# Optimization experiments

Measured on AMD Instinct MI355X. Metric: run time of the kernel, lower is better.

The kernel has to match this reference:

```python
import jax, jax.numpy as jnp
import numpy as np

NB, NC, NT = 64, 128, 6
NEURON = (25, 50, 100)
AXIS = 4
EPS = 1e-12


def _offdiag_idx(nc):
    # static [nc, nc-1] column indices of the off-diagonal entries per row
    idx = np.tile(np.arange(nc)[None, :], (nc, 1))
    mask = ~np.eye(nc, dtype=bool)
    return idx[mask].reshape(nc, nc - 1)


def setup_inputs() -> dict:
    key = jax.random.key(0)
    ks = jax.random.split(key, 8)
    P = NT * NT
    coords = jax.random.normal(ks[0], (NB, NC, 3), dtype=jnp.float32)
    atom_types = jax.random.randint(ks[1], (NC,), 0, NT)
    dims = [1] + list(NEURON)
    inp = {"coords": coords, "atom_types": atom_types}
    for i in range(3):
        bound = 1.0 / float(np.sqrt(dims[i]))
        inp[f"W{i+1}"] = jax.random.uniform(ks[2 + 2 * i], (P, dims[i + 1], dims[i]), jnp.float32, -bound, bound)
        inp[f"b{i+1}"] = jax.random.uniform(ks[3 + 2 * i], (P, dims[i + 1]), jnp.float32, -bound, bound)
    return inp


def _channel_dense(x, W, b, channels, res_mode):
    # x: [nb, Ppairs, in]; W[channels]: [Ppairs, out, in] (redundant per-pair gather, as in torch)
    y = jnp.einsum('bpi,poi->bpo', x, W[channels]) + b[channels]
    y = jnp.tanh(y)
    if res_mode == 1:
        y = y + x
    elif res_mode == 2:
        y = y + jnp.concatenate([x, x], axis=-1)
    return y


def _forward(coords, atom_types, W1, b1, W2, b2, W3, b3):
    nb, nc, _ = coords.shape
    idx = jnp.asarray(_offdiag_idx(nc))  # [nc, nc-1], static
    row = jnp.arange(nc)[:, None]

    rij = coords[:, :, None, :] - coords[:, None, :, :]          # [nb,nc,nc,3]
    rij = rij[:, row, idx]                                       # [nb,nc,nc-1,3] off-diagonal
    dij = jnp.linalg.norm(rij, axis=-1)                          # [nb,nc,nc-1]
    dinv = 1.0 / jnp.maximum(dij, EPS)
    loc_env_r = dinv
    loc_env_a = rij * (dinv * dinv)[..., None]                   # [nb,nc,nc-1,3]

    neighbor_types = atom_types[idx]                             # [nc,nc-1]
    channels = (atom_types[:, None] * NT + neighbor_types).reshape(-1)  # [nc*(nc-1)]

    x = loc_env_r.reshape(nb, -1, 1)                             # [nb,P,1]
    y = _channel_dense(x, W1, b1, channels, res_mode=0)          # 1 -> 25
    y = _channel_dense(y, W2, b2, channels, res_mode=2)          # 25 -> 50 (+concat res)
    y = _channel_dense(y, W3, b3, channels, res_mode=2)          # 50 -> 100 (+concat res)

    out = y.reshape(nb, nc, nc - 1, NEURON[-1])                  # [nb,nc,k,100]
    t1 = jnp.einsum('bnka,bnkf->bnaf', loc_env_a, out[..., :AXIS])   # [nb,nc,3,4]
    t2 = jnp.einsum('bnka,bnaf->bnkf', loc_env_a, t1)                # [nb,nc,k,4]
    res = jnp.einsum('bnkg,bnkf->bngf', out, t2)                     # [nb,nc,100,4]
    return res.reshape(nb, nc, -1)


def reference(coords, atom_types, W1, b1, W2, b2, W3, b3):
    return _forward(coords, atom_types, W1, b1, W2, b2, W3, b3)
```

## Files before the change

### kernel.cpp

```cpp
#include <hip/hip_runtime.h>

#define NBATCH 64
#define NCH    128
#define NTYPE  6
#define NK     127
#define N1     25
#define N2     50
#define N3     100
#define NAXIS  4
#define OUTPER 400
#define W2P    28
#define MAXKP  152
#define MAXC4  38

#define R5(M)  M(0) M(1) M(2) M(3) M(4)
#define R7(M)  M(0) M(1) M(2) M(3) M(4) M(5) M(6)
#define R12(M) M(0) M(1) M(2) M(3) M(4) M(5) M(6) M(7) M(8) M(9) M(10) M(11)
#define R25(M) M(0) M(1) M(2) M(3) M(4) M(5) M(6) M(7) M(8) M(9) M(10) M(11) M(12) \
               M(13) M(14) M(15) M(16) M(17) M(18) M(19) M(20) M(21) M(22) M(23) M(24)
#define R25A(M,a) M(a,0) M(a,1) M(a,2) M(a,3) M(a,4) M(a,5) M(a,6) M(a,7) M(a,8) M(a,9) \
               M(a,10) M(a,11) M(a,12) M(a,13) M(a,14) M(a,15) M(a,16) M(a,17) M(a,18) \
               M(a,19) M(a,20) M(a,21) M(a,22) M(a,23) M(a,24)
#define R50(M) R25(M) M(25) M(26) M(27) M(28) M(29) M(30) M(31) M(32) M(33) M(34) \
               M(35) M(36) M(37) M(38) M(39) M(40) M(41) M(42) M(43) M(44) M(45) \
               M(46) M(47) M(48) M(49)

__device__ __forceinline__ float tanh_fast(float x) {
    float e = __expf(2.0f * x);
    return 1.0f - 2.0f * __builtin_amdgcn_rcpf(e + 1.0f);
}

__global__ void k_transpose(const float* __restrict__ coords, float* __restrict__ ct) {
    int t = blockIdx.x * blockDim.x + threadIdx.x;
    if (t >= NBATCH * NCH * 3) return;
    int b  = t & (NBATCH - 1);
    int jd = t >> 6;
    int d  = jd % 3;
    int j  = jd / 3;
    ct[t] = coords[(b * NCH + j) * 3 + d];
}

__device__ __forceinline__ void sort_k_by_type(
    const int* __restrict__ types, int n, int* tysh, int* ks, int* bins, int tid, int nthr)
{
    for (int t = tid; t < NCH; t += nthr) tysh[t] = types[t];
    __syncthreads();
    if (tid == 0) {
        for (int t = 0; t < NTYPE; ++t) bins[t] = 0;
        for (int k = 0; k < NK; ++k) { int j = (k < n) ? k : k + 1; bins[tysh[j]]++; }
        int off = 0;
        for (int t = 0; t < NTYPE; ++t) { int c = bins[t]; bins[t] = off; off += c; }
        for (int k = 0; k < NK; ++k) { int j = (k < n) ? k : k + 1; ks[bins[tysh[j]]++] = k; }
    }
    __syncthreads();
}

__device__ __forceinline__ void sort_pad(
    const int* __restrict__ types, int n, int* tysh, int* ksp, int* chs, int* aux,
    int tid, int nthr)
{
    for (int t = tid; t < NCH; t += nthr) tysh[t] = types[t];
    __syncthreads();
    if (tid == 0) {
        int cnt[NTYPE], pos[NTYPE];
        for (int t = 0; t < NTYPE; ++t) cnt[t] = 0;
        for (int k = 0; k < NK; ++k) { int j = (k < n) ? k : k + 1; cnt[tysh[j]]++; }
        int c = 0;
        for (int t = 0; t < NTYPE; ++t) {
            pos[t] = c;
            int pc = (cnt[t] + 3) & ~3;
            for (int q = c >> 2; q < (c + pc) >> 2; ++q) chs[q] = t;
            for (int p = c + cnt[t]; p < c + pc; ++p) ksp[p] = -1;
            c += pc;
        }
        aux[0] = c >> 2;
        for (int k = 0; k < NK; ++k) { int j = (k < n) ? k : k + 1; ksp[pos[tysh[j]]++] = k; }
    }
    __syncthreads();
}

__global__ __launch_bounds__(256, 4) void k_mlp(
    const float* __restrict__ ct, const int* __restrict__ types,
    const float* __restrict__ W1, const float* __restrict__ B1,
    const float* __restrict__ W2, const float* __restrict__ B2,
    const float* __restrict__ W3, const float* __restrict__ B3,
    float* __restrict__ t1buf)
{
    __shared__ int ks[NK];
    __shared__ int tysh[NCH];
    __shared__ int bins[NTYPE];

    const int n  = blockIdx.x >> 2;
    const int qc = blockIdx.x & 3;
    const int w  = threadIdx.x >> 6;
    const int b  = threadIdx.x & 63;
    const int k0 = qc * 32 + w * 8;

    sort_k_by_type(types, n, tysh, ks, bins, threadIdx.x, 256);

    const float cx = ct[(n*3+0)*NBATCH + b];
    const float cy = ct[(n*3+1)*NBATCH + b];
    const float cz = ct[(n*3+2)*NBATCH + b];
    const int tn = __builtin_amdgcn_readfirstlane(tysh[n]);

    float t1a[12];
#define TIN(i) t1a[i] = 0.0f;
    R12(TIN)
#undef TIN

    for (int kk = 0; kk < 8; ++kk) {
        const int kidx = k0 + kk;
        if (kidx >= NK) break;
        const int sk = __builtin_amdgcn_readfirstlane(ks[kidx]);
        const int j  = (sk < n) ? sk : sk + 1;
        const int ch = __builtin_amdgcn_readfirstlane(tn * NTYPE + tysh[j]);

        const float dx = cx - ct[(j*3+0)*NBATCH + b];
        const float dy = cy - ct[(j*3+1)*NBATCH + b];
        const float dz = cz - ct[(j*3+2)*NBATCH + b];
        const float d2 = dx*dx + dy*dy + dz*dz;
        const float dd = sqrtf(d2);
        const float dinv = __builtin_amdgcn_rcpf(fmaxf(dd, 1e-12f));
        const float di2 = dinv * dinv;
        const float ax = dx * di2, ay = dy * di2, az = dz * di2;

        const float* w1r = W1 + ch * N1;
        const float* b1r = B1 + ch * N1;
        float y1[N1];
#define L1S(o) y1[o] = tanh_fast(fmaf(dinv, w1r[o], b1r[o]));
        R25(L1S)
#undef L1S

        const float* w2r = W2 + ch * (N2 * N1);
        const float* b2r = B2 + ch * N2;
        const float* w3r = W3 + ch * (N3 * N2);
        float zf[4];
        zf[0] = B3[ch*N3+0]; zf[1] = B3[ch*N3+1];
        zf[2] = B3[ch*N3+2]; zf[3] = B3[ch*N3+3];
        float r[4];
#define MLP2I(o,i) z = fmaf(w2r[(o)*N1+(i)], y1[i], z);
#define MLP2(o) { float z = b2r[o]; R25A(MLP2I,o) \
        float y2o = tanh_fast(z) + y1[(o)%N1]; \
        if ((o) < 4) r[(o)&3] = y2o; \
        zf[0] = fmaf(w3r[0*N2+(o)], y2o, zf[0]); \
        zf[1] = fmaf(w3r[1*N2+(o)], y2o, zf[1]); \
        zf[2] = fmaf(w3r[2*N2+(o)], y2o, zf[2]); \
        zf[3] = fmaf(w3r[3*N2+(o)], y2o, zf[3]); }
        R50(MLP2)
#undef MLP2
#undef MLP2I

#define O4F(f) { float o4 = tanh_fast(zf[f]) + r[f]; \
        t1a[0+(f)] = fmaf(ax, o4, t1a[0+(f)]); \
        t1a[4+(f)] = fmaf(ay, o4, t1a[4+(f)]); \
        t1a[8+(f)] = fmaf(az, o4, t1a[8+(f)]); }
        O4F(0) O4F(1) O4F(2) O4F(3)
#undef O4F
    }

    float* dst = t1buf + (n * 12) * NBATCH + b;
#define TAT(i) atomicAdd(dst + (i) * NBATCH, t1a[i]);
    R12(TAT)
#undef TAT
}

__global__ __launch_bounds__(512, 3) void k_res2(
    const float* __restrict__ ct, const int* __restrict__ types,
    const float* __restrict__ W1, const float* __restrict__ B1,
    const float* __restrict__ W2, const float* __restrict__ B2,
    const float* __restrict__ W3, const float* __restrict__ B3,
    const float* __restrict__ t1buf, float* __restrict__ out)
{
    __shared__ float y2t[4 * N2 * NBATCH];
    __shared__ float t2s[4 * NBATCH * NAXIS];
    __shared__ float w2s[N2 * W2P];
    __shared__ float w1s[N1], b1s[N1], b2s[N2];
    __shared__ int   ksp[MAXKP];
    __shared__ int   chs[MAXC4];
    __shared__ int   tysh[NCH];
    __shared__ int   aux[1];

    const int n    = blockIdx.x >> 2;
    const int gh   = (blockIdx.x >> 1) & 1;
    const int kh   = blockIdx.x & 1;
    const int w    = threadIdx.x >> 6;
    const int lane = threadIdx.x & 63;
    const int kk2  = w >> 1;
    const int h    = w & 1;
    const int tid  = threadIdx.x;

    sort_pad(types, n, tysh, ksp, chs, aux, tid, 512);
    const int nch4 = __builtin_amdgcn_readfirstlane(aux[0]);
    const int c_lo = kh ? (nch4 >> 1) : 0;
    const int c_hi = kh ? nch4 : (nch4 >> 1);

    const int tn = __builtin_amdgcn_readfirstlane(tysh[n]);

    float t1r[12];
#define T1L(i) t1r[i] = t1buf[(n*12 + (i))*NBATCH + lane];
    R12(T1L)
#undef T1L

    const int g0 = __builtin_amdgcn_readfirstlane(w * 7);
    int gg[7];
#define GGI(gi) gg[gi] = ((g0 + (gi)) < N2) ? (g0 + (gi)) : (N2 - 1);
    R7(GGI)
#undef GGI

    float racc[7][4];
#define RIN(gi) racc[gi][0]=0.f; racc[gi][1]=0.f; racc[gi][2]=0.f; racc[gi][3]=0.f;
    R7(RIN)
#undef RIN

    float b3v[7];
    int prevty = -1;

    for (int kc = c_lo; kc < c_hi; ++kc) {
        const int tj = __builtin_amdgcn_readfirstlane(chs[kc]);
        const int ch = tn * NTYPE + tj;
        if (tj != prevty) {
            for (int idx = tid; idx < N2*N1; idx += 512)
                w2s[(idx / N1) * W2P + (idx % N1)] = W2[ch*(N2*N1) + idx];
            if (tid < N1) { w1s[tid] = W1[ch*N1+tid]; b1s[tid] = B1[ch*N1+tid]; }
            if (tid < N2) b2s[tid] = B2[ch*N2+tid];
#define B3L(gi) b3v[gi] = B3[ch*N3 + gh*N2 + gg[gi]];
            R7(B3L)
#undef B3L
            prevty = tj;
            __syncthreads();
        }
        const int kb = kc * 4;
        {
            const int sk = __builtin_amdgcn_readfirstlane(ksp[kb + kk2]);
            if (sk >= 0) {
                const int j = (sk < n) ? sk : sk + 1;
                const float dx = ct[(n*3+0)*NBATCH + lane] - ct[(j*3+0)*NBATCH + lane];
                const float dy = ct[(n*3+1)*NBATCH + lane] - ct[(j*3+1)*NBATCH + lane];
                const float dz = ct[(n*3+2)*NBATCH + lane] - ct[(j*3+2)*NBATCH + lane];
                const float d2 = dx*dx + dy*dy + dz*dz;
                const float dd = sqrtf(d2);
                const float dinv = __builtin_amdgcn_rcpf(fmaxf(dd, 1e-12f));

                if (h == 0) {
                    const float di2 = dinv * dinv;
                    const float ax = dx * di2, ay = dy * di2, az = dz * di2;
#define T2W(f) t2s[(kk2*NBATCH + lane)*NAXIS + (f)] = \
                    ax*t1r[f] + ay*t1r[4+(f)] + az*t1r[8+(f)];
                    T2W(0) T2W(1) T2W(2) T2W(3)
#undef T2W
                }

                float y1[N1];
#define L1S(o) y1[o] = tanh_fast(fmaf(dinv, w1s[o], b1s[o]));
                R25(L1S)
#undef L1S
                const int ob = h * N1;
                float* y2w = &y2t[(kk2*N2 + ob)*NBATCH + lane];
#define P1Q(oi,q) { float4 wq = *(const float4*)&w2s[(ob+(oi))*W2P + (q)*4]; \
                    z = fmaf(wq.x, y1[(q)*4+0], z); z = fmaf(wq.y, y1[(q)*4+1], z); \
                    z = fmaf(wq.z, y1[(q)*4+2], z); z = fmaf(wq.w, y1[(q)*4+3], z); }
#define P1S(oi) { float z = b2s[ob+(oi)]; \
                  P1Q(oi,0) P1Q(oi,1) P1Q(oi,2) P1Q(oi,3) P1Q(oi,4) P1Q(oi,5) \
                  z = fmaf(w2s[(ob+(oi))*W2P + 24], y1[24], z); \
                  y2w[(oi)*NBATCH] = tanh_fast(z) + y1[oi]; }
                R25(P1S)
#undef P1S
#undef P1Q
            }
        }
        __syncthreads();
        const float* w3b = W3 + ch * (N3*N2) + (gh*N2) * N2;
        for (int kp = 0; kp < 2; ++kp) {
            const int skA = __builtin_amdgcn_readfirstlane(ksp[kb + kp*2 + 0]);
            const int skB = __builtin_amdgcn_readfirstlane(ksp[kb + kp*2 + 1]);
            if (skA < 0 && skB < 0) continue;
            const float* y2A = &y2t[((kp*2+0)*N2)*NBATCH + lane];
            const float* y2B = &y2t[((kp*2+1)*N2)*NBATCH + lane];
            float zA[7], zB[7];
#define ZIN(gi) zA[gi] = b3v[gi]; zB[gi] = b3v[gi];
            R7(ZIN)
#undef ZIN
            for (int ic = 0; ic < 10; ++ic) {
                const int io = ic * 5;
                float w35[7][5];
#define W35L(gi) w35[gi][0]=w3b[gg[gi]*N2+io+0]; w35[gi][1]=w3b[gg[gi]*N2+io+1]; \
                 w35[gi][2]=w3b[gg[gi]*N2+io+2]; w35[gi][3]=w3b[gg[gi]*N2+io+3]; \
                 w35[gi][4]=w3b[gg[gi]*N2+io+4];
                R7(W35L)
#undef W35L
                if (skA >= 0) {
                    float yv[5];
#define LDA(i) yv[i] = y2A[(io + (i))*NBATCH];
                    R5(LDA)
#undef LDA
#define FA(gi) zA[gi]=fmaf(w35[gi][0],yv[0],zA[gi]); zA[gi]=fmaf(w35[gi][1],yv[1],zA[gi]); \
               zA[gi]=fmaf(w35[gi][2],yv[2],zA[gi]); zA[gi]=fmaf(w35[gi][3],yv[3],zA[gi]); \
               zA[gi]=fmaf(w35[gi][4],yv[4],zA[gi]);
                    R7(FA)
#undef FA
                }
                if (skB >= 0) {
                    float yv[5];
#define LDB(i) yv[i] = y2B[(io + (i))*NBATCH];
                    R5(LDB)
#undef LDB
#define FB(gi) zB[gi]=fmaf(w35[gi][0],yv[0],zB[gi]); zB[gi]=fmaf(w35[gi][1],yv[1],zB[gi]); \
               zB[gi]=fmaf(w35[gi][2],yv[2],zB[gi]); zB[gi]=fmaf(w35[gi][3],yv[3],zB[gi]); \
               zB[gi]=fmaf(w35[gi][4],yv[4],zB[gi]);
                    R7(FB)
#undef FB
                }
            }
            if (skA >= 0) {
                const float4 t2v = *(const float4*)&t2s[((kp*2+0)*NBATCH + lane)*NAXIS];
#define PFA(gi) { float o3 = tanh_fast(zA[gi]) + y2A[gg[gi]*NBATCH]; \
                  racc[gi][0] = fmaf(o3, t2v.x, racc[gi][0]); \
                  racc[gi][1] = fmaf(o3, t2v.y, racc[gi][1]); \
                  racc[gi][2] = fmaf(o3, t2v.z, racc[gi][2]); \
                  racc[gi][3] = fmaf(o3, t2v.w, racc[gi][3]); }
                R7(PFA)
#undef PFA
            }
            if (skB >= 0) {
                const float4 t2v = *(const float4*)&t2s[((kp*2+1)*NBATCH + lane)*NAXIS];
#define PFB(gi) { float o3 = tanh_fast(zB[gi]) + y2B[gg[gi]*NBATCH]; \
                  racc[gi][0] = fmaf(o3, t2v.x, racc[gi][0]); \
                  racc[gi][1] = fmaf(o3, t2v.y, racc[gi][1]); \
                  racc[gi][2] = fmaf(o3, t2v.z, racc[gi][2]); \
                  racc[gi][3] = fmaf(o3, t2v.w, racc[gi][3]); }
                R7(PFB)
#undef PFB
            }
        }
        __syncthreads();
    }

#define PST(gi) if (g0 + (gi) < N2) { \
        float* dp = &out[(lane*NCH + n)*OUTPER + (gh*N2 + g0 + (gi))*NAXIS]; \
        atomicAdd(dp + 0, racc[gi][0]); \
        atomicAdd(dp + 1, racc[gi][1]); \
        atomicAdd(dp + 2, racc[gi][2]); \
        atomicAdd(dp + 3, racc[gi][3]); }
    R7(PST)
#undef PST
}

extern "C" void kernel_launch(void* const* d_in, const int* in_sizes, int n_in,
                              void* d_out, int out_size, void* d_ws, size_t ws_size,
                              hipStream_t stream) {
    const float* coords = (const float*)d_in[0];
    const int*   types  = (const int*)d_in[1];
    const float* W1 = (const float*)d_in[2];
    const float* B1 = (const float*)d_in[3];
    const float* W2 = (const float*)d_in[4];
    const float* B2 = (const float*)d_in[5];
    const float* W3 = (const float*)d_in[6];
    const float* B3 = (const float*)d_in[7];
    float* out = (float*)d_out;

    float* t1buf = (float*)d_ws;
    float* ct    = t1buf + NCH * 12 * NBATCH;

    hipMemsetAsync(t1buf, 0, (size_t)NCH * 12 * NBATCH * sizeof(float), stream);
    hipMemsetAsync(out, 0, (size_t)out_size * sizeof(float), stream);

    k_transpose<<<(NBATCH*NCH*3 + 255)/256, 256, 0, stream>>>(coords, ct);
    k_mlp <<<NCH*4, 256, 0, stream>>>(ct, types, W1,B1,W2,B2,W3,B3, t1buf);
    k_res2<<<NCH*4, 512, 0, stream>>>(ct, types, W1,B1,W2,B2,W3,B3, t1buf, out);
}
```

Measured before the change: 830.7 us.

## Stage per-channel weights in LDS for k_mlp and widen k_res2 to all outputs

k_mlp now uses the padded, type-sorted neighbour chunks from sort_pad. It loads W1/W2/B and the first four W3 rows into shared memory once per channel type, instead of reading them from global memory for every neighbour. k_res2 drops the two-way split over output halves and instead splits neighbours four ways per atom. It runs 12 waves per block covering all 100 outputs, with the concat residual indexed via rr. This removes the duplicated layer-2 recomputation across output halves. The cost is more registers per thread, four idle waves during the layer-2 phase, and an aggressive launch bound that may force register spills.

Result: slower. 1.147 ms (+38.1%).

```diff
diff --git a/kernel.cpp b/kernel.cpp
--- a/kernel.cpp
+++ b/kernel.cpp
@@ -10,11 +10,13 @@
 #define NAXIS  4
 #define OUTPER 400
 #define W2P    28
+#define W3P4   52
 #define MAXKP  152
 #define MAXC4  38
 
+#define R4(M)  M(0) M(1) M(2) M(3)
 #define R5(M)  M(0) M(1) M(2) M(3) M(4)
-#define R7(M)  M(0) M(1) M(2) M(3) M(4) M(5) M(6)
+#define R9(M)  M(0) M(1) M(2) M(3) M(4) M(5) M(6) M(7) M(8)
 #define R12(M) M(0) M(1) M(2) M(3) M(4) M(5) M(6) M(7) M(8) M(9) M(10) M(11)
 #define R25(M) M(0) M(1) M(2) M(3) M(4) M(5) M(6) M(7) M(8) M(9) M(10) M(11) M(12) \
                M(13) M(14) M(15) M(16) M(17) M(18) M(19) M(20) M(21) M(22) M(23) M(24)
@@ -38,21 +40,6 @@
     int d  = jd % 3;
     int j  = jd / 3;
     ct[t] = coords[(b * NCH + j) * 3 + d];
-}
-
-__device__ __forceinline__ void sort_k_by_type(
-    const int* __restrict__ types, int n, int* tysh, int* ks, int* bins, int tid, int nthr)
-{
-    for (int t = tid; t < NCH; t += nthr) tysh[t] = types[t];
-    __syncthreads();
-    if (tid == 0) {
-        for (int t = 0; t < NTYPE; ++t) bins[t] = 0;
-        for (int k = 0; k < NK; ++k) { int j = (k < n) ? k : k + 1; bins[tysh[j]]++; }
-        int off = 0;
-        for (int t = 0; t < NTYPE; ++t) { int c = bins[t]; bins[t] = off; off += c; }
-        for (int k = 0; k < NK; ++k) { int j = (k < n) ? k : k + 1; ks[bins[tysh[j]]++] = k; }
-    }
-    __syncthreads();
 }
 
 __device__ __forceinline__ void sort_pad(
@@ -86,34 +73,54 @@
     const float* __restrict__ W3, const float* __restrict__ B3,
     float* __restrict__ t1buf)
 {
-    __shared__ int ks[NK];
-    __shared__ int tysh[NCH];
-    __shared__ int bins[NTYPE];
-
-    const int n  = blockIdx.x >> 2;
-    const int qc = blockIdx.x & 3;
-    const int w  = threadIdx.x >> 6;
-    const int b  = threadIdx.x & 63;
-    const int k0 = qc * 32 + w * 8;
-
-    sort_k_by_type(types, n, tysh, ks, bins, threadIdx.x, 256);
-
+    __shared__ float w2s[N2 * W2P];
+    __shared__ float w3s4[4 * W3P4];
+    __shared__ float w1s[N1], b1s[N1], b2s[N2], b3s4[4];
+    __shared__ int   ksp[MAXKP];
+    __shared__ int   chs[MAXC4];
+    __shared__ int   tysh[NCH];
+    __shared__ int   aux[1];
+
+    const int n   = blockIdx.x >> 2;
+    const int qc  = blockIdx.x & 3;
+    const int w   = threadIdx.x >> 6;
+    const int b   = threadIdx.x & 63;
+    const int tid = threadIdx.x;
+
+    sort_pad(types, n, tysh, ksp, chs, aux, tid, 256);
+    const int nch4 = __builtin_amdgcn_readfirstlane(aux[0]);
+    const int c_lo = (qc * nch4) >> 2;
+    const int c_hi = ((qc + 1) * nch4) >> 2;
+
+    const int tn = __builtin_amdgcn_readfirstlane(tysh[n]);
     const float cx = ct[(n*3+0)*NBATCH + b];
     const float cy = ct[(n*3+1)*NBATCH + b];
     const float cz = ct[(n*3+2)*NBATCH + b];
-    const int tn = __builtin_amdgcn_readfirstlane(tysh[n]);
 
     float t1a[12];
 #define TIN(i) t1a[i] = 0.0f;
     R12(TIN)
 #undef TIN
 
-    for (int kk = 0; kk < 8; ++kk) {
-        const int kidx = k0 + kk;
-        if (kidx >= NK) break;
-        const int sk = __builtin_amdgcn_readfirstlane(ks[kidx]);
-        const int j  = (sk < n) ? sk : sk + 1;
-        const int ch = __builtin_amdgcn_readfirstlane(tn * NTYPE + tysh[j]);
+    int prevty = -1;
+    for (int kc = c_lo; kc < c_hi; ++kc) {
+        const int tj = __builtin_amdgcn_readfirstlane(chs[kc]);
+        const int ch = tn * NTYPE + tj;
+        if (tj != prevty) {
+            __syncthreads();
+            for (int idx = tid; idx < N2*N1; idx += 256)
+                w2s[(idx / N1) * W2P + (idx % N1)] = W2[ch*(N2*N1) + idx];
+            for (int idx = tid; idx < 4*N2; idx += 256)
+                w3s4[(idx / N2) * W3P4 + (idx % N2)] = W3[ch*(N3*N2) + idx];
+            if (tid < N1) { w1s[tid] = W1[ch*N1+tid]; b1s[tid] = B1[ch*N1+tid]; }
+            if (tid < N2) b2s[tid] = B2[ch*N2+tid];
+            if (tid < 4)  b3s4[tid] = B3[ch*N3+tid];
+            prevty = tj;
+            __syncthreads();
+        }
+        const int sk = __builtin_amdgcn_readfirstlane(ksp[kc*4 + w]);
+        if (sk < 0) continue;
+        const int j = (sk < n) ? sk : sk + 1;
 
         const float dx = cx - ct[(j*3+0)*NBATCH + b];
         const float dy = cy - ct[(j*3+1)*NBATCH + b];
@@ -124,33 +131,30 @@
         const float di2 = dinv * dinv;
         const float ax = dx * di2, ay = dy * di2, az = dz * di2;
 
-        const float* w1r = W1 + ch * N1;
-        const float* b1r = B1 + ch * N1;
         float y1[N1];
-#define L1S(o) y1[o] = tanh_fast(fmaf(dinv, w1r[o], b1r[o]));
+#define L1S(o) y1[o] = tanh_fast(fmaf(dinv, w1s[o], b1s[o]));
         R25(L1S)
 #undef L1S
 
-        const float* w2r = W2 + ch * (N2 * N1);
-        const float* b2r = B2 + ch * N2;
-        const float* w3r = W3 + ch * (N3 * N2);
-        float zf[4];
-        zf[0] = B3[ch*N3+0]; zf[1] = B3[ch*N3+1];
-        zf[2] = B3[ch*N3+2]; zf[3] = B3[ch*N3+3];
+        float zf0 = b3s4[0], zf1 = b3s4[1], zf2 = b3s4[2], zf3 = b3s4[3];
         float r[4];
-#define MLP2I(o,i) z = fmaf(w2r[(o)*N1+(i)], y1[i], z);
-#define MLP2(o) { float z = b2r[o]; R25A(MLP2I,o) \
-        float y2o = tanh_fast(z) + y1[(o)%N1]; \
-        if ((o) < 4) r[(o)&3] = y2o; \
-        zf[0] = fmaf(w3r[0*N2+(o)], y2o, zf[0]); \
-        zf[1] = fmaf(w3r[1*N2+(o)], y2o, zf[1]); \
-        zf[2] = fmaf(w3r[2*N2+(o)], y2o, zf[2]); \
-        zf[3] = fmaf(w3r[3*N2+(o)], y2o, zf[3]); }
+#define P1Q(o,q) { float4 wq = *(const float4*)&w2s[(o)*W2P + (q)*4]; \
+                   z = fmaf(wq.x, y1[(q)*4+0], z); z = fmaf(wq.y, y1[(q)*4+1], z); \
+                   z = fmaf(wq.z, y1[(q)*4+2], z); z = fmaf(wq.w, y1[(q)*4+3], z); }
+#define MLP2(o) { float z = b2s[o]; \
+                  P1Q(o,0) P1Q(o,1) P1Q(o,2) P1Q(o,3) P1Q(o,4) P1Q(o,5) \
+                  z = fmaf(w2s[(o)*W2P + 24], y1[24], z); \
+                  float y2o = tanh_fast(z) + y1[(o)%N1]; \
+                  if ((o) < 4) r[(o)&3] = y2o; \
+                  zf0 = fmaf(w3s4[0*W3P4+(o)], y2o, zf0); \
+                  zf1 = fmaf(w3s4[1*W3P4+(o)], y2o, zf1); \
+                  zf2 = fmaf(w3s4[2*W3P4+(o)], y2o, zf2); \
+                  zf3 = fmaf(w3s4[3*W3P4+(o)], y2o, zf3); }
         R50(MLP2)
 #undef MLP2
-#undef MLP2I
-
-#define O4F(f) { float o4 = tanh_fast(zf[f]) + r[f]; \
+#undef P1Q
+
+#define O4F(f) { float o4 = tanh_fast(f==0?zf0:f==1?zf1:f==2?zf2:zf3) + r[f]; \
         t1a[0+(f)] = fmaf(ax, o4, t1a[0+(f)]); \
         t1a[4+(f)] = fmaf(ay, o4, t1a[4+(f)]); \
         t1a[8+(f)] = fmaf(az, o4, t1a[8+(f)]); }
@@ -164,7 +168,7 @@
 #undef TAT
 }
 
-__global__ __launch_bounds__(512, 3) void k_res2(
+__global__ __launch_bounds__(768, 6) void k_res2(
     const float* __restrict__ ct, const int* __restrict__ types,
     const float* __restrict__ W1, const float* __restrict__ B1,
     const float* __restrict__ W2, const float* __restrict__ B2,
@@ -181,18 +185,17 @@
     __shared__ int   aux[1];
 
     const int n    = blockIdx.x >> 2;
-    const int gh   = (blockIdx.x >> 1) & 1;
-    const int kh   = blockIdx.x & 1;
+    const int kq   = blockIdx.x & 3;
     const int w    = threadIdx.x >> 6;
     const int lane = threadIdx.x & 63;
     const int kk2  = w >> 1;
     const int h    = w & 1;
     const int tid  = threadIdx.x;
 
-    sort_pad(types, n, tysh, ksp, chs, aux, tid, 512);
+    sort_pad(types, n, tysh, ksp, chs, aux, tid, 768);
     const int nch4 = __builtin_amdgcn_readfirstlane(aux[0]);
-    const int c_lo = kh ? (nch4 >> 1) : 0;
-    const int c_hi = kh ? nch4 : (nch4 >> 1);
+    const int c_lo = (kq * nch4) >> 2;
+    const int c_hi = ((kq + 1) * nch4) >> 2;
 
     const int tn = __builtin_amdgcn_readfirstlane(tysh[n]);
 
@@ -201,36 +204,37 @@
     R12(T1L)
 #undef T1L
 
-    const int g0 = __builtin_amdgcn_readfirstlane(w * 7);
-    int gg[7];
-#define GGI(gi) gg[gi] = ((g0 + (gi)) < N2) ? (g0 + (gi)) : (N2 - 1);
-    R7(GGI)
+    const int g0 = __builtin_amdgcn_readfirstlane(w * 9);
+    int gg[9], rr[9];
+#define GGI(gi) gg[gi] = ((g0 + (gi)) < N3) ? (g0 + (gi)) : (N3 - 1); \
+                rr[gi] = (gg[gi] >= N2) ? (gg[gi] - N2) : gg[gi];
+    R9(GGI)
 #undef GGI
 
-    float racc[7][4];
+    float racc[9][4];
 #define RIN(gi) racc[gi][0]=0.f; racc[gi][1]=0.f; racc[gi][2]=0.f; racc[gi][3]=0.f;
-    R7(RIN)
+    R9(RIN)
 #undef RIN
 
-    float b3v[7];
+    float b3v[9];
     int prevty = -1;
 
     for (int kc = c_lo; kc < c_hi; ++kc) {
         const int tj = __builtin_amdgcn_readfirstlane(chs[kc]);
         const int ch = tn * NTYPE + tj;
         if (tj != prevty) {
-            for (int idx = tid; idx < N2*N1; idx += 512)
+            for (int idx = tid; idx < N2*N1; idx += 768)
                 w2s[(idx / N1) * W2P + (idx % N1)] = W2[ch*(N2*N1) + idx];
             if (tid < N1) { w1s[tid] = W1[ch*N1+tid]; b1s[tid] = B1[ch*N1+tid]; }
             if (tid < N2) b2s[tid] = B2[ch*N2+tid];
-#define B3L(gi) b3v[gi] = B3[ch*N3 + gh*N2 + gg[gi]];
-            R7(B3L)
+#define B3L(gi) b3v[gi] = B3[ch*N3 + gg[gi]];
+            R9(B3L)
 #undef B3L
             prevty = tj;
             __syncthreads();
         }
         const int kb = kc * 4;
-        {
+        if (w < 8) {
             const int sk = __builtin_amdgcn_readfirstlane(ksp[kb + kk2]);
             if (sk >= 0) {
                 const int j = (sk < n) ? sk : sk + 1;
@@ -269,24 +273,24 @@
             }
         }
         __syncthreads();
-        const float* w3b = W3 + ch * (N3*N2) + (gh*N2) * N2;
+        const float* w3b = W3 + ch * (N3*N2);
         for (int kp = 0; kp < 2; ++kp) {
             const int skA = __builtin_amdgcn_readfirstlane(ksp[kb + kp*2 + 0]);
             const int skB = __builtin_amdgcn_readfirstlane(ksp[kb + kp*2 + 1]);
             if (skA < 0 && skB < 0) continue;
             const float* y2A = &y2t[((kp*2+0)*N2)*NBATCH + lane];
             const float* y2B = &y2t[((kp*2+1)*N2)*NBATCH + lane];
-            float zA[7], zB[7];
+            float zA[9], zB[9];
 #define ZIN(gi) zA[gi] = b3v[gi]; zB[gi] = b3v[gi];
-            R7(ZIN)
+            R9(ZIN)
 #undef ZIN
             for (int ic = 0; ic < 10; ++ic) {
                 const int io = ic * 5;
-                float w35[7][5];
+                float w35[9][5];
 #define W35L(gi) w35[gi][0]=w3b[gg[gi]*N2+io+0]; w35[gi][1]=w3b[gg[gi]*N2+io+1]; \
                  w35[gi][2]=w3b[gg[gi]*N2+io+2]; w35[gi][3]=w3b[gg[gi]*N2+io+3]; \
                  w35[gi][4]=w3b[gg[gi]*N2+io+4];
-                R7(W35L)
+                R9(W35L)
 #undef W35L
                 if (skA >= 0) {
                     float yv[5];
@@ -296,7 +300,7 @@
 #define FA(gi) zA[gi]=fmaf(w35[gi][0],yv[0],zA[gi]); zA[gi]=fmaf(w35[gi][1],yv[1],zA[gi]); \
                zA[gi]=fmaf(w35[gi][2],yv[2],zA[gi]); zA[gi]=fmaf(w35[gi][3],yv[3],zA[gi]); \
                zA[gi]=fmaf(w35[gi][4],yv[4],zA[gi]);
-                    R7(FA)
+                    R9(FA)
 #undef FA
                 }
                 if (skB >= 0) {
@@ -307,41 +311,41 @@
 #define FB(gi) zB[gi]=fmaf(w35[gi][0],yv[0],zB[gi]); zB[gi]=fmaf(w35[gi][1],yv[1],zB[gi]); \
                zB[gi]=fmaf(w35[gi][2],yv[2],zB[gi]); zB[gi]=fmaf(w35[gi][3],yv[3],zB[gi]); \
                zB[gi]=fmaf(w35[gi][4],yv[4],zB[gi]);
-                    R7(FB)
+                    R9(FB)
 #undef FB
                 }
             }
             if (skA >= 0) {
                 const float4 t2v = *(const float4*)&t2s[((kp*2+0)*NBATCH + lane)*NAXIS];
-#define PFA(gi) { float o3 = tanh_fast(zA[gi]) + y2A[gg[gi]*NBATCH]; \
+#define PFA(gi) { float o3 = tanh_fast(zA[gi]) + y2A[rr[gi]*NBATCH]; \
                   racc[gi][0] = fmaf(o3, t2v.x, racc[gi][0]); \
                   racc[gi][1] = fmaf(o3, t2v.y, racc[gi][1]); \
                   racc[gi][2] = fmaf(o3, t2v.z, racc[gi][2]); \
                   racc[gi][3] = fmaf(o3, t2v.w, racc[gi][3]); }
-                R7(PFA)
+                R9(PFA)
 #undef PFA
             }
             if (skB >= 0) {
                 const float4 t2v = *(const float4*)&t2s[((kp*2+1)*NBATCH + lane)*NAXIS];
-#define PFB(gi) { float o3 = tanh_fast(zB[gi]) + y2B[gg[gi]*NBATCH]; \
+#define PFB(gi) { float o3 = tanh_fast(zB[gi]) + y2B[rr[gi]*NBATCH]; \
                   racc[gi][0] = fmaf(o3, t2v.x, racc[gi][0]); \
                   racc[gi][1] = fmaf(o3, t2v.y, racc[gi][1]); \
                   racc[gi][2] = fmaf(o3, t2v.z, racc[gi][2]); \
                   racc[gi][3] = fmaf(o3, t2v.w, racc[gi][3]); }
-                R7(PFB)
+                R9(PFB)
 #undef PFB
             }
         }
         __syncthreads();
     }
 
-#define PST(gi) if (g0 + (gi) < N2) { \
-        float* dp = &out[(lane*NCH + n)*OUTPER + (gh*N2 + g0 + (gi))*NAXIS]; \
+#define PST(gi) if (g0 + (gi) < N3) { \
+        float* dp = &out[(lane*NCH + n)*OUTPER + gg[gi]*NAXIS]; \
         atomicAdd(dp + 0, racc[gi][0]); \
         atomicAdd(dp + 1, racc[gi][1]); \
         atomicAdd(dp + 2, racc[gi][2]); \
         atomicAdd(dp + 3, racc[gi][3]); }
-    R7(PST)
+    R9(PST)
 #undef PST
 }
 
@@ -366,5 +370,5 @@
 
     k_transpose<<<(NBATCH*NCH*3 + 255)/256, 256, 0, stream>>>(coords, ct);
     k_mlp <<<NCH*4, 256, 0, stream>>>(ct, types, W1,B1,W2,B2,W3,B3, t1buf);
-    k_res2<<<NCH*4, 512, 0, stream>>>(ct, types, W1,B1,W2,B2,W3,B3, t1buf, out);
-}
+    k_res2<<<NCH*4, 768, 0, stream>>>(ct, types, W1,B1,W2,B2,W3,B3, t1buf, out);
+}
```

## Split MLP work by padded type-chunks, drop shared W2 staging, halve res2 grid

Applied to the files above, without the earlier changes.

k_mlp now reuses the padded per-type sort and gives each wave one neighbor per chunk of four, so the channel index stays wave-uniform and weights come through scalar loads. k_res2 no longer stages W2/W1/B into shared memory; it reads them directly from global with uniform addresses, and it drops the k-half split so each block covers all chunks. The res2 grid is halved and launch bounds raised to 4 blocks per SM. The intent is to remove per-type reload barriers and shared-memory traffic. The costs are fewer blocks for parallelism and more scalar and global weight loads.

Measured after the change: 993.8 us. 19.6% more time.

```diff
diff --git a/kernel.cpp b/kernel.cpp
--- a/kernel.cpp
+++ b/kernel.cpp
@@ -9,7 +9,6 @@
 #define N3     100
 #define NAXIS  4
 #define OUTPER 400
-#define W2P    28
 #define MAXKP  152
 #define MAXC4  38
 
@@ -38,21 +37,6 @@
     int d  = jd % 3;
     int j  = jd / 3;
     ct[t] = coords[(b * NCH + j) * 3 + d];
-}
-
-__device__ __forceinline__ void sort_k_by_type(
-    const int* __restrict__ types, int n, int* tysh, int* ks, int* bins, int tid, int nthr)
-{
-    for (int t = tid; t < NCH; t += nthr) tysh[t] = types[t];
-    __syncthreads();
-    if (tid == 0) {
-        for (int t = 0; t < NTYPE; ++t) bins[t] = 0;
-        for (int k = 0; k < NK; ++k) { int j = (k < n) ? k : k + 1; bins[tysh[j]]++; }
-        int off = 0;
-        for (int t = 0; t < NTYPE; ++t) { int c = bins[t]; bins[t] = off; off += c; }
-        for (int k = 0; k < NK; ++k) { int j = (k < n) ? k : k + 1; ks[bins[tysh[j]]++] = k; }
-    }
-    __syncthreads();
 }
 
 __device__ __forceinline__ void sort_pad(
@@ -86,34 +70,37 @@
     const float* __restrict__ W3, const float* __restrict__ B3,
     float* __restrict__ t1buf)
 {
-    __shared__ int ks[NK];
+    __shared__ int ksp[MAXKP];
+    __shared__ int chs[MAXC4];
     __shared__ int tysh[NCH];
-    __shared__ int bins[NTYPE];
-
-    const int n  = blockIdx.x >> 2;
-    const int qc = blockIdx.x & 3;
-    const int w  = threadIdx.x >> 6;
-    const int b  = threadIdx.x & 63;
-    const int k0 = qc * 32 + w * 8;
-
-    sort_k_by_type(types, n, tysh, ks, bins, threadIdx.x, 256);
-
+    __shared__ int aux[1];
+
+    const int n   = blockIdx.x >> 2;
+    const int qc  = blockIdx.x & 3;
+    const int w   = threadIdx.x >> 6;
+    const int b   = threadIdx.x & 63;
+    const int tid = threadIdx.x;
+
+    sort_pad(types, n, tysh, ksp, chs, aux, tid, 256);
+    const int nch4 = __builtin_amdgcn_readfirstlane(aux[0]);
+    const int c_lo = (qc * nch4) >> 2;
+    const int c_hi = ((qc + 1) * nch4) >> 2;
+
+    const int tn = __builtin_amdgcn_readfirstlane(tysh[n]);
     const float cx = ct[(n*3+0)*NBATCH + b];
     const float cy = ct[(n*3+1)*NBATCH + b];
     const float cz = ct[(n*3+2)*NBATCH + b];
-    const int tn = __builtin_amdgcn_readfirstlane(tysh[n]);
 
     float t1a[12];
 #define TIN(i) t1a[i] = 0.0f;
     R12(TIN)
 #undef TIN
 
-    for (int kk = 0; kk < 8; ++kk) {
-        const int kidx = k0 + kk;
-        if (kidx >= NK) break;
-        const int sk = __builtin_amdgcn_readfirstlane(ks[kidx]);
-        const int j  = (sk < n) ? sk : sk + 1;
-        const int ch = __builtin_amdgcn_readfirstlane(tn * NTYPE + tysh[j]);
+    for (int kc = c_lo; kc < c_hi; ++kc) {
+        const int ch = tn * NTYPE + __builtin_amdgcn_readfirstlane(chs[kc]);
+        const int sk = __builtin_amdgcn_readfirstlane(ksp[kc*4 + w]);
+        if (sk < 0) continue;
+        const int j = (sk < n) ? sk : sk + 1;
 
         const float dx = cx - ct[(j*3+0)*NBATCH + b];
         const float dy = cy - ct[(j*3+1)*NBATCH + b];
@@ -134,23 +121,22 @@
         const float* w2r = W2 + ch * (N2 * N1);
         const float* b2r = B2 + ch * N2;
         const float* w3r = W3 + ch * (N3 * N2);
-        float zf[4];
-        zf[0] = B3[ch*N3+0]; zf[1] = B3[ch*N3+1];
-        zf[2] = B3[ch*N3+2]; zf[3] = B3[ch*N3+3];
+        float zf0 = B3[ch*N3+0], zf1 = B3[ch*N3+1];
+        float zf2 = B3[ch*N3+2], zf3 = B3[ch*N3+3];
         float r[4];
 #define MLP2I(o,i) z = fmaf(w2r[(o)*N1+(i)], y1[i], z);
 #define MLP2(o) { float z = b2r[o]; R25A(MLP2I,o) \
         float y2o = tanh_fast(z) + y1[(o)%N1]; \
         if ((o) < 4) r[(o)&3] = y2o; \
-        zf[0] = fmaf(w3r[0*N2+(o)], y2o, zf[0]); \
-        zf[1] = fmaf(w3r[1*N2+(o)], y2o, zf[1]); \
-        zf[2] = fmaf(w3r[2*N2+(o)], y2o, zf[2]); \
-        zf[3] = fmaf(w3r[3*N2+(o)], y2o, zf[3]); }
+        zf0 = fmaf(w3r[0*N2+(o)], y2o, zf0); \
+        zf1 = fmaf(w3r[1*N2+(o)], y2o, zf1); \
+        zf2 = fmaf(w3r[2*N2+(o)], y2o, zf2); \
+        zf3 = fmaf(w3r[3*N2+(o)], y2o, zf3); }
         R50(MLP2)
 #undef MLP2
 #undef MLP2I
 
-#define O4F(f) { float o4 = tanh_fast(zf[f]) + r[f]; \
+#define O4F(f) { float o4 = tanh_fast(f==0?zf0:f==1?zf1:f==2?zf2:zf3) + r[f]; \
         t1a[0+(f)] = fmaf(ax, o4, t1a[0+(f)]); \
         t1a[4+(f)] = fmaf(ay, o4, t1a[4+(f)]); \
         t1a[8+(f)] = fmaf(az, o4, t1a[8+(f)]); }
@@ -164,7 +150,7 @@
 #undef TAT
 }
 
-__global__ __launch_bounds__(512, 3) void k_res2(
+__global__ __launch_bounds__(512, 4) void k_res2(
     const float* __restrict__ ct, const int* __restrict__ types,
     const float* __restrict__ W1, const float* __restrict__ B1,
     const float* __restrict__ W2, const float* __restrict__ B2,
@@ -173,16 +159,13 @@
 {
     __shared__ float y2t[4 * N2 * NBATCH];
     __shared__ float t2s[4 * NBATCH * NAXIS];
-    __shared__ float w2s[N2 * W2P];
-    __shared__ float w1s[N1], b1s[N1], b2s[N2];
     __shared__ int   ksp[MAXKP];
     __shared__ int   chs[MAXC4];
     __shared__ int   tysh[NCH];
     __shared__ int   aux[1];
 
-    const int n    = blockIdx.x >> 2;
-    const int gh   = (blockIdx.x >> 1) & 1;
-    const int kh   = blockIdx.x & 1;
+    const int n    = blockIdx.x >> 1;
+    const int gh   = blockIdx.x & 1;
     const int w    = threadIdx.x >> 6;
     const int lane = threadIdx.x & 63;
     const int kk2  = w >> 1;
@@ -191,8 +174,6 @@
 
     sort_pad(types, n, tysh, ksp, chs, aux, tid, 512);
     const int nch4 = __builtin_amdgcn_readfirstlane(aux[0]);
-    const int c_lo = kh ? (nch4 >> 1) : 0;
-    const int c_hi = kh ? nch4 : (nch4 >> 1);
 
     const int tn = __builtin_amdgcn_readfirstlane(tysh[n]);
 
@@ -212,23 +193,12 @@
     R7(RIN)
 #undef RIN
 
-    float b3v[7];
-    int prevty = -1;
-
-    for (int kc = c_lo; kc < c_hi; ++kc) {
-        const int tj = __builtin_amdgcn_readfirstlane(chs[kc]);
-        const int ch = tn * NTYPE + tj;
-        if (tj != prevty) {
-            for (int idx = tid; idx < N2*N1; idx += 512)
-                w2s[(idx / N1) * W2P + (idx % N1)] = W2[ch*(N2*N1) + idx];
-            if (tid < N1) { w1s[tid] = W1[ch*N1+tid]; b1s[tid] = B1[ch*N1+tid]; }
-            if (tid < N2) b2s[tid] = B2[ch*N2+tid];
+    for (int kc = 0; kc < nch4; ++kc) {
+        const int ch = tn * NTYPE + __builtin_amdgcn_readfirstlane(chs[kc]);
+        float b3v[7];
 #define B3L(gi) b3v[gi] = B3[ch*N3 + gh*N2 + gg[gi]];
-            R7(B3L)
+        R7(B3L)
 #undef B3L
-            prevty = tj;
-            __syncthreads();
-        }
         const int kb = kc * 4;
         {
             const int sk = __builtin_amdgcn_readfirstlane(ksp[kb + kk2]);
@@ -250,22 +220,22 @@
 #undef T2W
                 }
 
+                const float* w1r = W1 + ch * N1;
+                const float* b1r = B1 + ch * N1;
                 float y1[N1];
-#define L1S(o) y1[o] = tanh_fast(fmaf(dinv, w1s[o], b1s[o]));
+#define L1S(o) y1[o] = tanh_fast(fmaf(dinv, w1r[o], b1r[o]));
                 R25(L1S)
 #undef L1S
                 const int ob = h * N1;
+                const float* w2h = W2 + ch * (N2*N1) + ob * N1;
+                const float* b2h = B2 + ch * N2 + ob;
                 float* y2w = &y2t[(kk2*N2 + ob)*NBATCH + lane];
-#define P1Q(oi,q) { float4 wq = *(const float4*)&w2s[(ob+(oi))*W2P + (q)*4]; \
-                    z = fmaf(wq.x, y1[(q)*4+0], z); z = fmaf(wq.y, y1[(q)*4+1], z); \
-                    z = fmaf(wq.z, y1[(q)*4+2], z); z = fmaf(wq.w, y1[(q)*4+3], z); }
-#define P1S(oi) { float z = b2s[ob+(oi)]; \
-                  P1Q(oi,0) P1Q(oi,1) P1Q(oi,2) P1Q(oi,3) P1Q(oi,4) P1Q(oi,5) \
-                  z = fmaf(w2s[(ob+(oi))*W2P + 24], y1[24], z); \
+#define P1I(oi,i) z = fmaf(w2h[(oi)*N1+(i)], y1[i], z);
+#define P1S(oi) { float z = b2h[oi]; R25A(P1I,oi) \
                   y2w[(oi)*NBATCH] = tanh_fast(z) + y1[oi]; }
                 R25(P1S)
 #undef P1S
-#undef P1Q
+#undef P1I
             }
         }
         __syncthreads();
@@ -366,5 +336,5 @@
 
     k_transpose<<<(NBATCH*NCH*3 + 255)/256, 256, 0, stream>>>(coords, ct);
     k_mlp <<<NCH*4, 256, 0, stream>>>(ct, types, W1,B1,W2,B2,W3,B3, t1buf);
-    k_res2<<<NCH*4, 512, 0, stream>>>(ct, types, W1,B1,W2,B2,W3,B3, t1buf, out);
-}
+    k_res2<<<NCH*2, 512, 0, stream>>>(ct, types, W1,B1,W2,B2,W3,B3, t1buf, out);
+}
```
